# Kernel tuning notes

Measured on AMD Instinct MI355X. Metric: run time of the kernel, lower is better.

The kernel has to match this reference:

```python
import jax, jax.numpy as jnp
import numpy as np
from jax import lax

B = 16        # point clouds per batch
NPC = 4096    # points per cloud (N = B*NPC = 65536)
M_PC = 1024   # centroids per cloud after FPS (ratio=0.25)
K = 64        # max_num_neighbors (hardcoded in module)
R = 0.2       # radius
F_IN = 64     # input feature dim


def _fps(p, m):
    """Farthest point sampling on p:[n,3] -> m int32 indices (deterministic, start at 0)."""
    n = p.shape[0]
    def step(carry, _):
        d, last = carry
        nd = jnp.minimum(d, jnp.sum((p - p[last]) ** 2, axis=-1))
        return (nd, jnp.argmax(nd).astype(jnp.int32)), last
    (_, _), idxs = lax.scan(step, (jnp.full((n,), jnp.inf, p.dtype), jnp.int32(0)), None, length=m)
    return idxs


def setup_inputs() -> dict:
    key = jax.random.key(0)
    k0, k1, k2, k3 = jax.random.split(key, 4)
    N = B * NPC
    x = jax.random.normal(k0, (N, F_IN), jnp.float32)
    pos = jax.random.uniform(k1, (N, 3), jnp.float32)  # unit cube -> r=0.2 balls are well populated
    batch = jnp.repeat(jnp.arange(B, dtype=jnp.int32), NPC)
    W1 = jax.random.normal(k2, (F_IN + 3, 64), jnp.float32) * 0.1
    b1 = jnp.zeros((64,), jnp.float32)
    W2 = jax.random.normal(k3, (64, 128), jnp.float32) * 0.1
    b2 = jnp.zeros((128,), jnp.float32)
    return {"x": x, "pos": pos, "batch": batch, "W1": W1, "b1": b1, "W2": W2, "b2": b2}


def reference(x, pos, batch, W1, b1, W2, b2):
    pos_b = pos.reshape(B, NPC, 3)
    x_b = x.reshape(B, NPC, F_IN)

    # 1. FPS sampling per cloud -> centroid indices [B, M_PC]
    idx = jax.vmap(lambda p: _fps(p, M_PC))(pos_b)
    pos_c = jnp.take_along_axis(pos_b, idx[:, :, None], axis=1)  # [B,M,3]

    # 2. radius neighbor search: K nearest within R per centroid (same cloud only)
    d2 = jnp.sum((pos_c[:, :, None, :] - pos_b[:, None, :, :]) ** 2, axis=-1)  # [B,M,NPC]
    neg, nidx = lax.top_k(-d2, K)           # K smallest distances
    valid = (-neg) <= R * R                 # [B,M,K] inside-ball mask

    # 3. PointNetConv: gather, per-edge MLP on [x_j, pos_j - pos_i], max-aggregate
    x_j = jax.vmap(lambda xb, ib: xb[ib])(x_b, nidx)    # [B,M,K,F_IN]
    p_j = jax.vmap(lambda pb, ib: pb[ib])(pos_b, nidx)  # [B,M,K,3]
    rel = p_j - pos_c[:, :, None, :]
    feat = jnp.concatenate([x_j, rel], axis=-1)          # [B,M,K,F_IN+3]
    h = jax.nn.relu(feat @ W1 + b1)
    h = h @ W2 + b2                                      # plain last layer (PyG MLP default)
    h = jnp.where(valid[..., None], h, -jnp.inf)
    out = jnp.max(h, axis=2)                             # [B,M,128]
    out = jnp.where(jnp.any(valid, axis=2)[..., None], out, 0.0)

    out = out.reshape(B * M_PC, -1)
    pos_out = pos_c.reshape(B * M_PC, 3)
    batch_out = jnp.repeat(jnp.arange(B, dtype=batch.dtype), M_PC)
    return out, pos_out, batch_out
```

## Files before the change

### kernel.cpp

```cpp
#include <hip/hip_runtime.h>

#define NB   16
#define NPC  4096
#define MPC  1024
#define KNB  64
#define FIN  64
#define CAP  448

typedef unsigned short u16;
typedef unsigned int   u32;
typedef unsigned long long u64;
typedef __attribute__((ext_vector_type(8))) short short8;
typedef __attribute__((ext_vector_type(4))) float f32x4;

__device__ __forceinline__ u16 f2bf(float f) {
  u32 u = __float_as_uint(f);
  u = u + 0x7fffu + ((u >> 16) & 1u);
  return (u16)(u >> 16);
}
__device__ __forceinline__ float bf2f(u16 b) {
  return __uint_as_float(((u32)b) << 16);
}

#define DPP64_MAX(best, ctrl, rmask) do { \
  u32 _lo = (u32)(best), _hi = (u32)((best) >> 32); \
  u32 _olo = (u32)__builtin_amdgcn_update_dpp((int)_lo, (int)_lo, (ctrl), (rmask), 0xf, false); \
  u32 _ohi = (u32)__builtin_amdgcn_update_dpp((int)_hi, (int)_hi, (ctrl), (rmask), 0xf, false); \
  u64 _o = ((u64)_ohi << 32) | _olo; \
  (best) = _o > (best) ? _o : (best); \
} while (0)

__device__ __forceinline__ u32 wave_max_u32(u32 x) {
  u32 t;
  t = (u32)__builtin_amdgcn_update_dpp((int)x, (int)x, 0x111, 0xf, 0xf, false); x = x > t ? x : t;
  t = (u32)__builtin_amdgcn_update_dpp((int)x, (int)x, 0x112, 0xf, 0xf, false); x = x > t ? x : t;
  t = (u32)__builtin_amdgcn_update_dpp((int)x, (int)x, 0x114, 0xf, 0xf, false); x = x > t ? x : t;
  t = (u32)__builtin_amdgcn_update_dpp((int)x, (int)x, 0x118, 0xf, 0xf, false); x = x > t ? x : t;
  t = (u32)__builtin_amdgcn_update_dpp((int)x, (int)x, 0x142, 0xa, 0xf, false); x = x > t ? x : t;
  t = (u32)__builtin_amdgcn_update_dpp((int)x, (int)x, 0x143, 0xc, 0xf, false); x = x > t ? x : t;
  return x;
}
__device__ __forceinline__ u32 wave_min_u32(u32 x) {
  u32 t;
  t = (u32)__builtin_amdgcn_update_dpp((int)x, (int)x, 0x111, 0xf, 0xf, false); x = x < t ? x : t;
  t = (u32)__builtin_amdgcn_update_dpp((int)x, (int)x, 0x112, 0xf, 0xf, false); x = x < t ? x : t;
  t = (u32)__builtin_amdgcn_update_dpp((int)x, (int)x, 0x114, 0xf, 0xf, false); x = x < t ? x : t;
  t = (u32)__builtin_amdgcn_update_dpp((int)x, (int)x, 0x118, 0xf, 0xf, false); x = x < t ? x : t;
  t = (u32)__builtin_amdgcn_update_dpp((int)x, (int)x, 0x142, 0xa, 0xf, false); x = x < t ? x : t;
  t = (u32)__builtin_amdgcn_update_dpp((int)x, (int)x, 0x143, 0xc, 0xf, false); x = x < t ? x : t;
  return x;
}

struct FpsLDS {
  float4 sxyz[NPC];
  u64 swave[2][8];
  int sidx[MPC];
};
struct YLDS { float xs[64][68]; float ws[64][68]; };
union FusedLDS { FpsLDS f; YLDS g; char pad[86016]; };

__global__ __launch_bounds__(512)
void fused_kernel(const float* __restrict__ pos, const float* __restrict__ x,
                  const float* __restrict__ w1, const float* __restrict__ w2,
                  int* __restrict__ idx_out, float* __restrict__ pos_out,
                  float* __restrict__ batch_out, u16* __restrict__ y,
                  u16* __restrict__ w2t) {
  __shared__ FusedLDS L;
  const int bid = blockIdx.x;
  const int t = threadIdx.x;
  if (bid < NB) {
    const int b = bid;
    const int w = t >> 6, lane = t & 63;
    const float* P = pos + (size_t)b * NPC * 3;
    for (int i = t; i < NPC; i += 512)
      L.f.sxyz[i] = make_float4(P[3*i+0], P[3*i+1], P[3*i+2], 0.f);
    for (int i = t; i < MPC; i += 512) batch_out[b*MPC + i] = (float)b;
    if (t == 0) L.f.sidx[0] = 0;
    __syncthreads();
    float px[8], py[8], pz[8], mind[8];
#pragma unroll
    for (int r = 0; r < 8; ++r) {
      float4 p = L.f.sxyz[t + (r << 9)];
      px[r] = p.x; py[r] = p.y; pz[r] = p.z;
      mind[r] = __builtin_inff();
    }
    int last = 0;
    for (int m = 1; m < MPC; ++m) {
      float4 c = L.f.sxyz[last];
      u32 vmax = 0;
#pragma unroll
      for (int r = 0; r < 8; ++r) {
        float dx = __fsub_rn(px[r], c.x);
        float dy = __fsub_rn(py[r], c.y);
        float dz = __fsub_rn(pz[r], c.z);
        float d2 = __fadd_rn(__fadd_rn(__fmul_rn(dx,dx), __fmul_rn(dy,dy)), __fmul_rn(dz,dz));
        mind[r] = fminf(mind[r], d2);
        u32 bits = __float_as_uint(mind[r]);
        vmax = bits > vmax ? bits : vmax;
      }
      vmax = wave_max_u32(vmax);
      u32 V = (u32)__builtin_amdgcn_readlane((int)vmax, 63);
      u32 cand = 0xffffffffu;
#pragma unroll
      for (int r = 7; r >= 0; --r)
        cand = (__float_as_uint(mind[r]) == V) ? (u32)(t + (r << 9)) : cand;
      cand = wave_min_u32(cand);
      if (lane == 63) L.f.swave[m & 1][w] = ((u64)V << 32) | (u32)(~cand);
      __syncthreads();
      u64 sv = 0;
      if (lane < 8) sv = L.f.swave[m & 1][lane];
      DPP64_MAX(sv, 0x111, 0xf);
      DPP64_MAX(sv, 0x112, 0xf);
      DPP64_MAX(sv, 0x114, 0xf);
      u32 lo = (u32)__builtin_amdgcn_readlane((int)(u32)sv, 7);
      last = (int)(~lo);
      if (t == 0) L.f.sidx[m] = last;
    }
    __syncthreads();
    for (int i = t; i < MPC; i += 512) {
      int ii = L.f.sidx[i];
      idx_out[b*MPC + i] = ii;
      float4 p = L.f.sxyz[ii];
      size_t po = ((size_t)b*MPC + i)*3;
      pos_out[po+0] = p.x; pos_out[po+1] = p.y; pos_out[po+2] = p.z;
    }
  } else if (bid < NB + 1024) {
    const size_t row0 = (size_t)(bid - NB) * 64;
#pragma unroll
    for (int k = 0; k < 2; ++k) {
      int l4 = t + 512*k;
      int r = l4 >> 4, c4 = l4 & 15;
      *(float4*)&L.g.xs[r][c4*4] = *(const float4*)&x[(row0 + r)*64 + c4*4];
      *(float4*)&L.g.ws[r][c4*4] = *(const float4*)&w1[r*64 + c4*4];
    }
    __syncthreads();
    const int r = t >> 3, c0 = (t & 7) << 3;
    float acc[8];
#pragma unroll
    for (int i = 0; i < 8; ++i) acc[i] = 0.f;
    for (int k = 0; k < 64; ++k) {
      float a = L.g.xs[r][k];
      float4 w0 = *(const float4*)&L.g.ws[k][c0];
      float4 w1v = *(const float4*)&L.g.ws[k][c0 + 4];
      acc[0] += a * w0.x; acc[1] += a * w0.y; acc[2] += a * w0.z; acc[3] += a * w0.w;
      acc[4] += a * w1v.x; acc[5] += a * w1v.y; acc[6] += a * w1v.z; acc[7] += a * w1v.w;
    }
    u32 u[4];
#pragma unroll
    for (int i = 0; i < 4; ++i)
      u[i] = (u32)f2bf(acc[2*i]) | ((u32)f2bf(acc[2*i+1]) << 16);
    *(uint4*)(y + ((row0 + r)*64 + c0)) = make_uint4(u[0], u[1], u[2], u[3]);
  } else {
    for (int i = t; i < 64*128; i += 512) {
      int k = i >> 7, c = i & 127;
      w2t[c*64 + k] = f2bf(w2[i]);
    }
  }
}

__global__ __launch_bounds__(256)
void nbr_kernel(const float* __restrict__ pos, const int* __restrict__ idx,
                int* __restrict__ nbr, int* __restrict__ nvalid) {
  const int bid = blockIdx.x;
  const int sw = (bid & 7) * 512 + (bid >> 3);
  const int cloud = sw >> 8;
  const int mbase = (sw & 255) << 2;
  __shared__ float sx[NPC], sy[NPC], sz[NPC];
  __shared__ u64 cand[4][CAP];
  const float* P = pos + (size_t)cloud * NPC * 3;
  const int t = threadIdx.x;
  for (int i = t; i < NPC; i += 256) { sx[i]=P[3*i]; sy[i]=P[3*i+1]; sz[i]=P[3*i+2]; }
  __syncthreads();
  const int wv = t >> 6, lane = t & 63;
  const int m = mbase + wv;
  const int g = cloud * MPC + m;
  const int ci = idx[g];
  const float cx = sx[ci], cy = sy[ci], cz = sz[ci];
  const float R2 = 0.04000000059604644775f;
  const u64 ltmask = (lane == 0) ? 0ull : (~0ull >> (64 - lane));
  int base = 0;
  for (int i = 0; i < NPC/64; ++i) {
    int j = (i << 6) + lane;
    float dx = __fsub_rn(cx, sx[j]);
    float dy = __fsub_rn(cy, sy[j]);
    float dz = __fsub_rn(cz, sz[j]);
    float d2 = __fadd_rn(__fadd_rn(__fmul_rn(dx,dx), __fmul_rn(dy,dy)), __fmul_rn(dz,dz));
    bool in = d2 <= R2;
    u64 mk = __ballot(in);
    if (in) {
      int slot = base + (int)__popcll(mk & ltmask);
      if (slot < CAP)
        cand[wv][slot] = ((u64)__float_as_uint(d2) << 32) | (u32)j;
    }
    base += (int)__popcll(mk);
  }
  int cnt = base < CAP ? base : CAP;
  u64 mykey[7];
  int myrank[7];
#pragma unroll
  for (int u = 0; u < 7; ++u) {
    int s = lane + (u << 6);
    mykey[u] = (s < cnt) ? cand[wv][s] : ~0ull;
    myrank[u] = 0;
  }
  for (int jj = 0; jj < cnt; ++jj) {
    u64 kj = cand[wv][jj];
#pragma unroll
    for (int u = 0; u < 7; ++u) myrank[u] += (kj < mykey[u]) ? 1 : 0;
  }
#pragma unroll
  for (int u = 0; u < 7; ++u) {
    int s = lane + (u << 6);
    if (s < cnt && myrank[u] < KNB)
      nbr[(size_t)g*KNB + myrank[u]] = cloud*NPC + (int)(mykey[u] & 0xffffffffull);
  }
  if (lane == 0) nvalid[g] = cnt < KNB ? cnt : KNB;
}

__global__ __launch_bounds__(256)
void conv_kernel(const float* __restrict__ pos, const int* __restrict__ idx,
                 const int* __restrict__ nbr, const int* __restrict__ nvalid,
                 const u16* __restrict__ y, const u16* __restrict__ w2t,
                 const float* __restrict__ w1, const float* __restrict__ b1,
                 const float* __restrict__ b2, float* __restrict__ out) {
  const int bid = blockIdx.x;
  const int g = (bid & 7) * 2048 + (bid >> 3);
  const int cloud = g >> 10;
  __shared__ u16 YH[64][72];
  __shared__ u16 WT[128][72];
  __shared__ float rel[64][3];
  __shared__ int nbs[64];
  __shared__ float w1p[192];
  __shared__ float b1s[64];
  const int t = threadIdx.x;
  const int nv = nvalid[g];
  if (t < 64) nbs[t] = (t < nv) ? nbr[(size_t)g*KNB + t] : -1;
  if (t < 192) w1p[t] = w1[64*64 + t];
  else         b1s[t - 192] = b1[t - 192];
  __syncthreads();
  if (t < 64) {
    int ci = cloud*NPC + idx[g];
    float cxx = pos[3*ci], cyy = pos[3*ci+1], czz = pos[3*ci+2];
    int j = nbs[t];
    float r0 = 0.f, r1 = 0.f, r2 = 0.f;
    if (t < nv && j >= 0) {
      r0 = pos[3*j]   - cxx;
      r1 = pos[3*j+1] - cyy;
      r2 = pos[3*j+2] - czz;
    }
    rel[t][0] = r0; rel[t][1] = r1; rel[t][2] = r2;
  }
  {
    int row = t >> 2, part = t & 3;
    int j = nbs[row];
    uint4 v0 = make_uint4(0,0,0,0), v1 = make_uint4(0,0,0,0);
    if (row < nv && j >= 0) {
      const uint4* src = (const uint4*)(y + (size_t)j*64);
      v0 = src[part*2]; v1 = src[part*2 + 1];
    }
    *(uint4*)&YH[row][part*16]     = v0;
    *(uint4*)&YH[row][part*16 + 8] = v1;
  }
#pragma unroll
  for (int k = 0; k < 4; ++k) {
    int l = t + 256*k;
    int row = l >> 3, part = l & 7;
    *(uint4*)&WT[row][part*8] = ((const uint4*)w2t)[l];
  }
  __syncthreads();
  {
    int s = t >> 2, c0 = (t & 3) << 4;
    float rx = rel[s][0], ry = rel[s][1], rz = rel[s][2];
#pragma unroll
    for (int c = 0; c < 16; ++c) {
      int cc = c0 + c;
      float v = bf2f(YH[s][cc]) + rx*w1p[cc] + ry*w1p[64+cc] + rz*w1p[128+cc] + b1s[cc];
      v = fmaxf(v, 0.f);
      YH[s][cc] = f2bf(v);
    }
  }
  __syncthreads();
  const int wv = t >> 6, lane = t & 63;
  const int arow = lane & 15, agrp = lane >> 4;
  const int col0 = wv << 5;
  f32x4 acc[4][2];
#pragma unroll
  for (int mt = 0; mt < 4; ++mt)
#pragma unroll
    for (int nt = 0; nt < 2; ++nt) {
      f32x4 z = {0.f, 0.f, 0.f, 0.f};
      acc[mt][nt] = z;
    }
#pragma unroll
  for (int kk = 0; kk < 2; ++kk) {
    short8 a[4], bm[2];
#pragma unroll
    for (int mt = 0; mt < 4; ++mt)
      a[mt] = *(const short8*)&YH[mt*16 + arow][kk*32 + agrp*8];
#pragma unroll
    for (int nt = 0; nt < 2; ++nt)
      bm[nt] = *(const short8*)&WT[col0 + nt*16 + arow][kk*32 + agrp*8];
#pragma unroll
    for (int mt = 0; mt < 4; ++mt)
#pragma unroll
      for (int nt = 0; nt < 2; ++nt)
        acc[mt][nt] = __builtin_amdgcn_mfma_f32_16x16x32_bf16(a[mt], bm[nt], acc[mt][nt], 0, 0, 0);
  }
  float p0 = -__builtin_inff(), p1 = -__builtin_inff();
#pragma unroll
  for (int mt = 0; mt < 4; ++mt) {
#pragma unroll
    for (int r = 0; r < 4; ++r) {
      int slot = mt*16 + agrp*4 + r;
      if (slot < nv) {
        p0 = fmaxf(p0, acc[mt][0][r]);
        p1 = fmaxf(p1, acc[mt][1][r]);
      }
    }
  }
  p0 = fmaxf(p0, __shfl_xor(p0, 16, 64));
  p0 = fmaxf(p0, __shfl_xor(p0, 32, 64));
  p1 = fmaxf(p1, __shfl_xor(p1, 16, 64));
  p1 = fmaxf(p1, __shfl_xor(p1, 32, 64));
  if (lane < 16) {
    int c = col0 + lane;
    out[(size_t)g*128 + c]      = (nv > 0) ? p0 + b2[c]      : 0.f;
    out[(size_t)g*128 + c + 16] = (nv > 0) ? p1 + b2[c + 16] : 0.f;
  }
}

extern "C" void kernel_launch(void* const* d_in, const int* in_sizes, int n_in,
                              void* d_out, int out_size, void* d_ws, size_t ws_size,
                              hipStream_t stream) {
  const float* x   = (const float*)d_in[0];
  const float* pos = (const float*)d_in[1];
  const float* W1  = (const float*)d_in[3];
  const float* b1  = (const float*)d_in[4];
  const float* W2  = (const float*)d_in[5];
  const float* b2  = (const float*)d_in[6];

  float* out       = (float*)d_out;
  float* pos_out   = out + (size_t)NB*MPC*128;
  float* batch_out = pos_out + (size_t)NB*MPC*3;

  char* ws = (char*)d_ws;
  int* idx    = (int*)(ws);
  int* nvalid = (int*)(ws + 65536);
  int* nbr    = (int*)(ws + 131072);
  u16* w2t    = (u16*)(ws + 131072 + 4194304);
  u16* y      = (u16*)(ws + 131072 + 4194304 + 16384);

  fused_kernel<<<NB + 1024 + 1, 512, 0, stream>>>(pos, x, W1, W2, idx, pos_out,
                                                  batch_out, y, w2t);
  nbr_kernel <<<4096,  256,  0, stream>>>(pos, idx, nbr, nvalid);
  conv_kernel<<<16384, 256,  0, stream>>>(pos, idx, nbr, nvalid, y, w2t, W1, b1, b2, out);
}
```

Before: 893.6 us.

## Fuse neighbor search and PointNet conv into one kernel with shared-memory handoff

Merges the radius-neighbor kernel and the conv kernel into a single kernel. Each block finds neighbors for four centroids, keeps neighbor indices and relative positions in shared memory, then runs the MLP and max-reduce for each centroid in turn. A union reuses the position staging buffers for the conv tiles. This removes the global nbr/nvalid round trip and one launch, but the conv phase now runs serially over four centroids per block with more barriers and fewer blocks.

```diff
diff --git a/kernel.cpp b/kernel.cpp
--- a/kernel.cpp
+++ b/kernel.cpp
@@ -158,174 +158,169 @@
   }
 }
 
+struct NCStage { float sx[NPC], sy[NPC], sz[NPC]; };
+struct NCConv  { u16 YH[64][72]; u16 WT[128][72]; };
+union  NCU     { NCStage s; NCConv c; };
+
 __global__ __launch_bounds__(256)
-void nbr_kernel(const float* __restrict__ pos, const int* __restrict__ idx,
-                int* __restrict__ nbr, int* __restrict__ nvalid) {
+void nbrconv_kernel(const float* __restrict__ pos, const int* __restrict__ idx,
+                    const u16* __restrict__ y, const u16* __restrict__ w2t,
+                    const float* __restrict__ w1, const float* __restrict__ b1,
+                    const float* __restrict__ b2, float* __restrict__ out) {
+  __shared__ NCU  L;
+  __shared__ u64  cand[4][CAP];
+  __shared__ float rel[4][64][3];
+  __shared__ int   nbs[4][64];
+  __shared__ int   nvs[4];
+  __shared__ float w1p[192];
+  __shared__ float b1s[64];
   const int bid = blockIdx.x;
   const int sw = (bid & 7) * 512 + (bid >> 3);
   const int cloud = sw >> 8;
   const int mbase = (sw & 255) << 2;
-  __shared__ float sx[NPC], sy[NPC], sz[NPC];
-  __shared__ u64 cand[4][CAP];
+  const int t = threadIdx.x;
   const float* P = pos + (size_t)cloud * NPC * 3;
-  const int t = threadIdx.x;
-  for (int i = t; i < NPC; i += 256) { sx[i]=P[3*i]; sy[i]=P[3*i+1]; sz[i]=P[3*i+2]; }
-  __syncthreads();
-  const int wv = t >> 6, lane = t & 63;
-  const int m = mbase + wv;
-  const int g = cloud * MPC + m;
-  const int ci = idx[g];
-  const float cx = sx[ci], cy = sy[ci], cz = sz[ci];
-  const float R2 = 0.04000000059604644775f;
-  const u64 ltmask = (lane == 0) ? 0ull : (~0ull >> (64 - lane));
-  int base = 0;
-  for (int i = 0; i < NPC/64; ++i) {
-    int j = (i << 6) + lane;
-    float dx = __fsub_rn(cx, sx[j]);
-    float dy = __fsub_rn(cy, sy[j]);
-    float dz = __fsub_rn(cz, sz[j]);
-    float d2 = __fadd_rn(__fadd_rn(__fmul_rn(dx,dx), __fmul_rn(dy,dy)), __fmul_rn(dz,dz));
-    bool in = d2 <= R2;
-    u64 mk = __ballot(in);
-    if (in) {
-      int slot = base + (int)__popcll(mk & ltmask);
-      if (slot < CAP)
-        cand[wv][slot] = ((u64)__float_as_uint(d2) << 32) | (u32)j;
-    }
-    base += (int)__popcll(mk);
-  }
-  int cnt = base < CAP ? base : CAP;
-  u64 mykey[7];
-  int myrank[7];
-#pragma unroll
-  for (int u = 0; u < 7; ++u) {
-    int s = lane + (u << 6);
-    mykey[u] = (s < cnt) ? cand[wv][s] : ~0ull;
-    myrank[u] = 0;
-  }
-  for (int jj = 0; jj < cnt; ++jj) {
-    u64 kj = cand[wv][jj];
-#pragma unroll
-    for (int u = 0; u < 7; ++u) myrank[u] += (kj < mykey[u]) ? 1 : 0;
-  }
-#pragma unroll
-  for (int u = 0; u < 7; ++u) {
-    int s = lane + (u << 6);
-    if (s < cnt && myrank[u] < KNB)
-      nbr[(size_t)g*KNB + myrank[u]] = cloud*NPC + (int)(mykey[u] & 0xffffffffull);
-  }
-  if (lane == 0) nvalid[g] = cnt < KNB ? cnt : KNB;
-}
-
-__global__ __launch_bounds__(256)
-void conv_kernel(const float* __restrict__ pos, const int* __restrict__ idx,
-                 const int* __restrict__ nbr, const int* __restrict__ nvalid,
-                 const u16* __restrict__ y, const u16* __restrict__ w2t,
-                 const float* __restrict__ w1, const float* __restrict__ b1,
-                 const float* __restrict__ b2, float* __restrict__ out) {
-  const int bid = blockIdx.x;
-  const int g = (bid & 7) * 2048 + (bid >> 3);
-  const int cloud = g >> 10;
-  __shared__ u16 YH[64][72];
-  __shared__ u16 WT[128][72];
-  __shared__ float rel[64][3];
-  __shared__ int nbs[64];
-  __shared__ float w1p[192];
-  __shared__ float b1s[64];
-  const int t = threadIdx.x;
-  const int nv = nvalid[g];
-  if (t < 64) nbs[t] = (t < nv) ? nbr[(size_t)g*KNB + t] : -1;
+  for (int i = t; i < NPC; i += 256) { L.s.sx[i]=P[3*i]; L.s.sy[i]=P[3*i+1]; L.s.sz[i]=P[3*i+2]; }
+  {
+    int w0_ = t >> 6, l0_ = t & 63;
+    nbs[w0_][l0_] = -1;
+    rel[w0_][l0_][0] = 0.f; rel[w0_][l0_][1] = 0.f; rel[w0_][l0_][2] = 0.f;
+  }
   if (t < 192) w1p[t] = w1[64*64 + t];
   else         b1s[t - 192] = b1[t - 192];
   __syncthreads();
-  if (t < 64) {
-    int ci = cloud*NPC + idx[g];
-    float cxx = pos[3*ci], cyy = pos[3*ci+1], czz = pos[3*ci+2];
-    int j = nbs[t];
-    float r0 = 0.f, r1 = 0.f, r2 = 0.f;
-    if (t < nv && j >= 0) {
-      r0 = pos[3*j]   - cxx;
-      r1 = pos[3*j+1] - cyy;
-      r2 = pos[3*j+2] - czz;
-    }
-    rel[t][0] = r0; rel[t][1] = r1; rel[t][2] = r2;
-  }
   {
-    int row = t >> 2, part = t & 3;
-    int j = nbs[row];
-    uint4 v0 = make_uint4(0,0,0,0), v1 = make_uint4(0,0,0,0);
-    if (row < nv && j >= 0) {
-      const uint4* src = (const uint4*)(y + (size_t)j*64);
-      v0 = src[part*2]; v1 = src[part*2 + 1];
-    }
-    *(uint4*)&YH[row][part*16]     = v0;
-    *(uint4*)&YH[row][part*16 + 8] = v1;
-  }
+    const int wv = t >> 6, lane = t & 63;
+    const int g = cloud * MPC + mbase + wv;
+    const int ci = idx[g];
+    const float cx = L.s.sx[ci], cy = L.s.sy[ci], cz = L.s.sz[ci];
+    const float R2 = 0.04000000059604644775f;
+    const u64 ltmask = (lane == 0) ? 0ull : (~0ull >> (64 - lane));
+    int base = 0;
+    for (int i = 0; i < NPC/64; ++i) {
+      int j = (i << 6) + lane;
+      float dx = __fsub_rn(cx, L.s.sx[j]);
+      float dy = __fsub_rn(cy, L.s.sy[j]);
+      float dz = __fsub_rn(cz, L.s.sz[j]);
+      float d2 = __fadd_rn(__fadd_rn(__fmul_rn(dx,dx), __fmul_rn(dy,dy)), __fmul_rn(dz,dz));
+      bool in = d2 <= R2;
+      u64 mk = __ballot(in);
+      if (in) {
+        int slot = base + (int)__popcll(mk & ltmask);
+        if (slot < CAP)
+          cand[wv][slot] = ((u64)__float_as_uint(d2) << 32) | (u32)j;
+      }
+      base += (int)__popcll(mk);
+    }
+    int cnt = base < CAP ? base : CAP;
+    u64 mykey[7];
+    int myrank[7];
+#pragma unroll
+    for (int u = 0; u < 7; ++u) {
+      int s = lane + (u << 6);
+      mykey[u] = (s < cnt) ? cand[wv][s] : ~0ull;
+      myrank[u] = 0;
+    }
+    for (int jj = 0; jj < cnt; ++jj) {
+      u64 kj = cand[wv][jj];
+#pragma unroll
+      for (int u = 0; u < 7; ++u) myrank[u] += (kj < mykey[u]) ? 1 : 0;
+    }
+#pragma unroll
+    for (int u = 0; u < 7; ++u) {
+      int s = lane + (u << 6);
+      if (s < cnt && myrank[u] < KNB) {
+        int j = (int)(mykey[u] & 0xffffffffull);
+        nbs[wv][myrank[u]] = cloud*NPC + j;
+        rel[wv][myrank[u]][0] = L.s.sx[j] - cx;
+        rel[wv][myrank[u]][1] = L.s.sy[j] - cy;
+        rel[wv][myrank[u]][2] = L.s.sz[j] - cz;
+      }
+    }
+    if (lane == 0) nvs[wv] = cnt < KNB ? cnt : KNB;
+  }
+  __syncthreads();
 #pragma unroll
   for (int k = 0; k < 4; ++k) {
     int l = t + 256*k;
     int row = l >> 3, part = l & 7;
-    *(uint4*)&WT[row][part*8] = ((const uint4*)w2t)[l];
-  }
-  __syncthreads();
-  {
-    int s = t >> 2, c0 = (t & 3) << 4;
-    float rx = rel[s][0], ry = rel[s][1], rz = rel[s][2];
-#pragma unroll
-    for (int c = 0; c < 16; ++c) {
-      int cc = c0 + c;
-      float v = bf2f(YH[s][cc]) + rx*w1p[cc] + ry*w1p[64+cc] + rz*w1p[128+cc] + b1s[cc];
-      v = fmaxf(v, 0.f);
-      YH[s][cc] = f2bf(v);
-    }
-  }
-  __syncthreads();
-  const int wv = t >> 6, lane = t & 63;
-  const int arow = lane & 15, agrp = lane >> 4;
-  const int col0 = wv << 5;
-  f32x4 acc[4][2];
-#pragma unroll
-  for (int mt = 0; mt < 4; ++mt)
-#pragma unroll
-    for (int nt = 0; nt < 2; ++nt) {
-      f32x4 z = {0.f, 0.f, 0.f, 0.f};
-      acc[mt][nt] = z;
-    }
-#pragma unroll
-  for (int kk = 0; kk < 2; ++kk) {
-    short8 a[4], bm[2];
+    *(uint4*)&L.c.WT[row][part*8] = ((const uint4*)w2t)[l];
+  }
+  for (int k = 0; k < 4; ++k) {
+    const int g = cloud*MPC + mbase + k;
+    const int nv = nvs[k];
+    if (k > 0) __syncthreads();
+    {
+      int row = t >> 2, part = t & 3;
+      int j = nbs[k][row];
+      uint4 v0 = make_uint4(0,0,0,0), v1 = make_uint4(0,0,0,0);
+      if (j >= 0) {
+        const uint4* src = (const uint4*)(y + (size_t)j*64);
+        v0 = src[part*2]; v1 = src[part*2 + 1];
+      }
+      *(uint4*)&L.c.YH[row][part*16]     = v0;
+      *(uint4*)&L.c.YH[row][part*16 + 8] = v1;
+    }
+    __syncthreads();
+    {
+      int s = t >> 2, c0 = (t & 3) << 4;
+      float rx = rel[k][s][0], ry = rel[k][s][1], rz = rel[k][s][2];
+#pragma unroll
+      for (int c = 0; c < 16; ++c) {
+        int cc = c0 + c;
+        float v = bf2f(L.c.YH[s][cc]) + rx*w1p[cc] + ry*w1p[64+cc] + rz*w1p[128+cc] + b1s[cc];
+        v = fmaxf(v, 0.f);
+        L.c.YH[s][cc] = f2bf(v);
+      }
+    }
+    __syncthreads();
+    const int wv = t >> 6, lane = t & 63;
+    const int arow = lane & 15, agrp = lane >> 4;
+    const int col0 = wv << 5;
+    f32x4 acc[4][2];
 #pragma unroll
     for (int mt = 0; mt < 4; ++mt)
-      a[mt] = *(const short8*)&YH[mt*16 + arow][kk*32 + agrp*8];
-#pragma unroll
-    for (int nt = 0; nt < 2; ++nt)
-      bm[nt] = *(const short8*)&WT[col0 + nt*16 + arow][kk*32 + agrp*8];
-#pragma unroll
-    for (int mt = 0; mt < 4; ++mt)
+#pragma unroll
+      for (int nt = 0; nt < 2; ++nt) {
+        f32x4 z = {0.f, 0.f, 0.f, 0.f};
+        acc[mt][nt] = z;
+      }
+#pragma unroll
+    for (int kk = 0; kk < 2; ++kk) {
+      short8 a[4], bm[2];
+#pragma unroll
+      for (int mt = 0; mt < 4; ++mt)
+        a[mt] = *(const short8*)&L.c.YH[mt*16 + arow][kk*32 + agrp*8];
 #pragma unroll
       for (int nt = 0; nt < 2; ++nt)
-        acc[mt][nt] = __builtin_amdgcn_mfma_f32_16x16x32_bf16(a[mt], bm[nt], acc[mt][nt], 0, 0, 0);
-  }
-  float p0 = -__builtin_inff(), p1 = -__builtin_inff();
-#pragma unroll
-  for (int mt = 0; mt < 4; ++mt) {
-#pragma unroll
-    for (int r = 0; r < 4; ++r) {
-      int slot = mt*16 + agrp*4 + r;
-      if (slot < nv) {
-        p0 = fmaxf(p0, acc[mt][0][r]);
-        p1 = fmaxf(p1, acc[mt][1][r]);
-      }
-    }
-  }
-  p0 = fmaxf(p0, __shfl_xor(p0, 16, 64));
-  p0 = fmaxf(p0, __shfl_xor(p0, 32, 64));
-  p1 = fmaxf(p1, __shfl_xor(p1, 16, 64));
-  p1 = fmaxf(p1, __shfl_xor(p1, 32, 64));
-  if (lane < 16) {
-    int c = col0 + lane;
-    out[(size_t)g*128 + c]      = (nv > 0) ? p0 + b2[c]      : 0.f;
-    out[(size_t)g*128 + c + 16] = (nv > 0) ? p1 + b2[c + 16] : 0.f;
+        bm[nt] = *(const short8*)&L.c.WT[col0 + nt*16 + arow][kk*32 + agrp*8];
+#pragma unroll
+      for (int mt = 0; mt < 4; ++mt)
+#pragma unroll
+        for (int nt = 0; nt < 2; ++nt)
+          acc[mt][nt] = __builtin_amdgcn_mfma_f32_16x16x32_bf16(a[mt], bm[nt], acc[mt][nt], 0, 0, 0);
+    }
+    float p0 = -__builtin_inff(), p1 = -__builtin_inff();
+#pragma unroll
+    for (int mt = 0; mt < 4; ++mt) {
+#pragma unroll
+      for (int r = 0; r < 4; ++r) {
+        int slot = mt*16 + agrp*4 + r;
+        if (slot < nv) {
+          p0 = fmaxf(p0, acc[mt][0][r]);
+          p1 = fmaxf(p1, acc[mt][1][r]);
+        }
+      }
+    }
+    p0 = fmaxf(p0, __shfl_xor(p0, 16, 64));
+    p0 = fmaxf(p0, __shfl_xor(p0, 32, 64));
+    p1 = fmaxf(p1, __shfl_xor(p1, 16, 64));
+    p1 = fmaxf(p1, __shfl_xor(p1, 32, 64));
+    if (lane < 16) {
+      int c = col0 + lane;
+      out[(size_t)g*128 + c]      = (nv > 0) ? p0 + b2[c]      : 0.f;
+      out[(size_t)g*128 + c + 16] = (nv > 0) ? p1 + b2[c + 16] : 0.f;
+    }
   }
 }
 
@@ -344,14 +339,11 @@
   float* batch_out = pos_out + (size_t)NB*MPC*3;
 
   char* ws = (char*)d_ws;
-  int* idx    = (int*)(ws);
-  int* nvalid = (int*)(ws + 65536);
-  int* nbr    = (int*)(ws + 131072);
-  u16* w2t    = (u16*)(ws + 131072 + 4194304);
-  u16* y      = (u16*)(ws + 131072 + 4194304 + 16384);
-
-  fused_kernel<<<NB + 1024 + 1, 512, 0, stream>>>(pos, x, W1, W2, idx, pos_out,
-                                                  batch_out, y, w2t);
-  nbr_kernel <<<4096,  256,  0, stream>>>(pos, idx, nbr, nvalid);
-  conv_kernel<<<16384, 256,  0, stream>>>(pos, idx, nbr, nvalid, y, w2t, W1, b1, b2, out);
-}
+  int* idx  = (int*)(ws);
+  u16* w2t  = (u16*)(ws + 65536);
+  u16* y    = (u16*)(ws + 65536 + 16384);
+
+  fused_kernel  <<<NB + 1024 + 1, 512, 0, stream>>>(pos, x, W1, W2, idx, pos_out,
+                                                    batch_out, y, w2t);
+  nbrconv_kernel<<<4096, 256, 0, stream>>>(pos, idx, y, w2t, W1, b1, b2, out);
+}
```

Result: slower. 927.6 us (+3.8%).

## Process two point clouds per FPS block to amortize per-iteration barrier latency

Applied to the files above, without the earlier changes.

Each FPS block now runs farthest-point sampling for two clouds at once, interleaving their distance updates and wave reductions and sharing one __syncthreads per iteration. The serial FPS loop is latency-bound by the block barrier and the DPP reduction chains, so two independent chains per block should hide that latency and halve the barrier count per cloud. The cost is double the register and LDS use per block (about 128KB LDS), which lowers occupancy, and only 8 FPS blocks are launched instead of 16.

```diff
diff --git a/kernel.cpp b/kernel.cpp
--- a/kernel.cpp
+++ b/kernel.cpp
@@ -51,13 +51,14 @@
   return x;
 }
 
-struct FpsLDS {
-  float4 sxyz[NPC];
-  u64 swave[2][8];
-  int sidx[MPC];
+struct FpsLDS2 {
+  float4 sA[NPC];
+  float4 sB[NPC];
+  u64 swA[2][8], swB[2][8];
+  int siA[MPC], siB[MPC];
 };
 struct YLDS { float xs[64][68]; float ws[64][68]; };
-union FusedLDS { FpsLDS f; YLDS g; char pad[86016]; };
+union FusedLDS { FpsLDS2 f; YLDS g; };
 
 __global__ __launch_bounds__(512)
 void fused_kernel(const float* __restrict__ pos, const float* __restrict__ x,
@@ -68,64 +69,94 @@
   __shared__ FusedLDS L;
   const int bid = blockIdx.x;
   const int t = threadIdx.x;
-  if (bid < NB) {
-    const int b = bid;
+  if (bid < 8) {
+    const int cA = 2*bid, cB = 2*bid + 1;
     const int w = t >> 6, lane = t & 63;
-    const float* P = pos + (size_t)b * NPC * 3;
-    for (int i = t; i < NPC; i += 512)
-      L.f.sxyz[i] = make_float4(P[3*i+0], P[3*i+1], P[3*i+2], 0.f);
-    for (int i = t; i < MPC; i += 512) batch_out[b*MPC + i] = (float)b;
-    if (t == 0) L.f.sidx[0] = 0;
+    const float* PA = pos + (size_t)cA * NPC * 3;
+    const float* PB = pos + (size_t)cB * NPC * 3;
+    for (int i = t; i < NPC; i += 512) {
+      L.f.sA[i] = make_float4(PA[3*i+0], PA[3*i+1], PA[3*i+2], 0.f);
+      L.f.sB[i] = make_float4(PB[3*i+0], PB[3*i+1], PB[3*i+2], 0.f);
+    }
+    for (int i = t; i < MPC; i += 512) {
+      batch_out[cA*MPC + i] = (float)cA;
+      batch_out[cB*MPC + i] = (float)cB;
+    }
+    if (t == 0) { L.f.siA[0] = 0; L.f.siB[0] = 0; }
     __syncthreads();
-    float px[8], py[8], pz[8], mind[8];
+    float pxA[8], pyA[8], pzA[8], mindA[8];
+    float pxB[8], pyB[8], pzB[8], mindB[8];
 #pragma unroll
     for (int r = 0; r < 8; ++r) {
-      float4 p = L.f.sxyz[t + (r << 9)];
-      px[r] = p.x; py[r] = p.y; pz[r] = p.z;
-      mind[r] = __builtin_inff();
-    }
-    int last = 0;
+      float4 a = L.f.sA[t + (r << 9)];
+      float4 b = L.f.sB[t + (r << 9)];
+      pxA[r] = a.x; pyA[r] = a.y; pzA[r] = a.z; mindA[r] = __builtin_inff();
+      pxB[r] = b.x; pyB[r] = b.y; pzB[r] = b.z; mindB[r] = __builtin_inff();
+    }
+    int lastA = 0, lastB = 0;
     for (int m = 1; m < MPC; ++m) {
-      float4 c = L.f.sxyz[last];
-      u32 vmax = 0;
+      const int pr = m & 1;
+      float4 ca = L.f.sA[lastA];
+      float4 cb = L.f.sB[lastB];
+      u32 vmaxA = 0, vmaxB = 0;
 #pragma unroll
       for (int r = 0; r < 8; ++r) {
-        float dx = __fsub_rn(px[r], c.x);
-        float dy = __fsub_rn(py[r], c.y);
-        float dz = __fsub_rn(pz[r], c.z);
-        float d2 = __fadd_rn(__fadd_rn(__fmul_rn(dx,dx), __fmul_rn(dy,dy)), __fmul_rn(dz,dz));
-        mind[r] = fminf(mind[r], d2);
-        u32 bits = __float_as_uint(mind[r]);
-        vmax = bits > vmax ? bits : vmax;
+        float dxA = __fsub_rn(pxA[r], ca.x);
+        float dyA = __fsub_rn(pyA[r], ca.y);
+        float dzA = __fsub_rn(pzA[r], ca.z);
+        float d2A = __fadd_rn(__fadd_rn(__fmul_rn(dxA,dxA), __fmul_rn(dyA,dyA)), __fmul_rn(dzA,dzA));
+        mindA[r] = fminf(mindA[r], d2A);
+        u32 bA = __float_as_uint(mindA[r]);
+        vmaxA = bA > vmaxA ? bA : vmaxA;
+        float dxB = __fsub_rn(pxB[r], cb.x);
+        float dyB = __fsub_rn(pyB[r], cb.y);
+        float dzB = __fsub_rn(pzB[r], cb.z);
+        float d2B = __fadd_rn(__fadd_rn(__fmul_rn(dxB,dxB), __fmul_rn(dyB,dyB)), __fmul_rn(dzB,dzB));
+        mindB[r] = fminf(mindB[r], d2B);
+        u32 bB = __float_as_uint(mindB[r]);
+        vmaxB = bB > vmaxB ? bB : vmaxB;
       }
-      vmax = wave_max_u32(vmax);
-      u32 V = (u32)__builtin_amdgcn_readlane((int)vmax, 63);
-      u32 cand = 0xffffffffu;
-#pragma unroll
-      for (int r = 7; r >= 0; --r)
-        cand = (__float_as_uint(mind[r]) == V) ? (u32)(t + (r << 9)) : cand;
-      cand = wave_min_u32(cand);
-      if (lane == 63) L.f.swave[m & 1][w] = ((u64)V << 32) | (u32)(~cand);
+      vmaxA = wave_max_u32(vmaxA);
+      vmaxB = wave_max_u32(vmaxB);
+      u32 VA = (u32)__builtin_amdgcn_readlane((int)vmaxA, 63);
+      u32 VB = (u32)__builtin_amdgcn_readlane((int)vmaxB, 63);
+      u32 candA = 0xffffffffu, candB = 0xffffffffu;
+#pragma unroll
+      for (int r = 7; r >= 0; --r) {
+        candA = (__float_as_uint(mindA[r]) == VA) ? (u32)(t + (r << 9)) : candA;
+        candB = (__float_as_uint(mindB[r]) == VB) ? (u32)(t + (r << 9)) : candB;
+      }
+      candA = wave_min_u32(candA);
+      candB = wave_min_u32(candB);
+      if (lane == 63) {
+        L.f.swA[pr][w] = ((u64)VA << 32) | (u32)(~candA);
+        L.f.swB[pr][w] = ((u64)VB << 32) | (u32)(~candB);
+      }
       __syncthreads();
       u64 sv = 0;
-      if (lane < 8) sv = L.f.swave[m & 1][lane];
+      if (lane < 8) sv = L.f.swA[pr][lane];
+      else if (lane >= 16 && lane < 24) sv = L.f.swB[pr][lane - 16];
       DPP64_MAX(sv, 0x111, 0xf);
       DPP64_MAX(sv, 0x112, 0xf);
       DPP64_MAX(sv, 0x114, 0xf);
-      u32 lo = (u32)__builtin_amdgcn_readlane((int)(u32)sv, 7);
-      last = (int)(~lo);
-      if (t == 0) L.f.sidx[m] = last;
+      u32 loA = (u32)__builtin_amdgcn_readlane((int)(u32)sv, 7);
+      u32 loB = (u32)__builtin_amdgcn_readlane((int)(u32)sv, 23);
+      lastA = (int)(~loA);
+      lastB = (int)(~loB);
+      if (t == 0) { L.f.siA[m] = lastA; L.f.siB[m] = lastB; }
     }
     __syncthreads();
     for (int i = t; i < MPC; i += 512) {
-      int ii = L.f.sidx[i];
-      idx_out[b*MPC + i] = ii;
-      float4 p = L.f.sxyz[ii];
-      size_t po = ((size_t)b*MPC + i)*3;
-      pos_out[po+0] = p.x; pos_out[po+1] = p.y; pos_out[po+2] = p.z;
-    }
-  } else if (bid < NB + 1024) {
-    const size_t row0 = (size_t)(bid - NB) * 64;
+      int ia = L.f.siA[i], ib = L.f.siB[i];
+      idx_out[cA*MPC + i] = ia;
+      idx_out[cB*MPC + i] = ib;
+      float4 pa = L.f.sA[ia], pb = L.f.sB[ib];
+      size_t poA = ((size_t)cA*MPC + i)*3, poB = ((size_t)cB*MPC + i)*3;
+      pos_out[poA+0] = pa.x; pos_out[poA+1] = pa.y; pos_out[poA+2] = pa.z;
+      pos_out[poB+0] = pb.x; pos_out[poB+1] = pb.y; pos_out[poB+2] = pb.z;
+    }
+  } else if (bid < 8 + 1024) {
+    const size_t row0 = (size_t)(bid - 8) * 64;
 #pragma unroll
     for (int k = 0; k < 2; ++k) {
       int l4 = t + 512*k;
@@ -350,8 +381,8 @@
   u16* w2t    = (u16*)(ws + 131072 + 4194304);
   u16* y      = (u16*)(ws + 131072 + 4194304 + 16384);
 
-  fused_kernel<<<NB + 1024 + 1, 512, 0, stream>>>(pos, x, W1, W2, idx, pos_out,
-                                                  batch_out, y, w2t);
-  nbr_kernel <<<4096,  256,  0, stream>>>(pos, idx, nbr, nvalid);
-  conv_kernel<<<16384, 256,  0, stream>>>(pos, idx, nbr, nvalid, y, w2t, W1, b1, b2, out);
-}
+  fused_kernel<<<8 + 1024 + 1, 512, 0, stream>>>(pos, x, W1, W2, idx, pos_out,
+                                                 batch_out, y, w2t);
+  nbr_kernel <<<4096,  256, 0, stream>>>(pos, idx, nbr, nvalid);
+  conv_kernel<<<16384, 256, 0, stream>>>(pos, idx, nbr, nvalid, y, w2t, W1, b1, b2, out);
+}
```

Result: slower. 1.334 ms (+49.3%).
